# Kernel optimization log

Measured on AMD Instinct MI355X. Metric: run time of the kernel, lower is better.

## Reference

```python
import jax, jax.numpy as jnp
import numpy as np

N, D, H, E, K = 4096, 512, 2048, 8, 2  # tokens, input/output dim, expert hidden, num_experts, top_k


def setup_inputs() -> dict:
    key = jax.random.key(0)
    k_x, k_r, k_w1, k_b1, k_w2, k_b2 = jax.random.split(key, 6)
    input_batch = jax.random.normal(k_x, (N, D), dtype=jnp.float32)
    # Router-style top-k selection: guarantees the K expert ids per token are distinct
    # (required by the torch nonzero-based dispatch) and probabilities are a softmax
    # over the selected logits, matching a standard MoE sampler.
    router_logits = jax.random.normal(k_r, (N, E), dtype=jnp.float32)
    top_vals, top_idx = jax.lax.top_k(router_logits, K)
    probabilities = jax.nn.softmax(top_vals, axis=-1)            # [N, K]
    indices = top_idx.astype(jnp.int64)                          # [N, K]
    scale = 0.02
    W1 = scale * jax.random.normal(k_w1, (E, D, H), dtype=jnp.float32)
    b1 = jnp.zeros((E, H), dtype=jnp.float32)
    W2 = scale * jax.random.normal(k_w2, (E, H, D), dtype=jnp.float32)
    b2 = jnp.zeros((E, D), dtype=jnp.float32)
    return {"input_batch": input_batch, "probabilities": probabilities, "indices": indices,
            "W1": W1, "b1": b1, "W2": W2, "b2": b2}


def reference(input_batch, probabilities, indices, W1, b1, W2, b2):
    # Each expert is a dense 2-layer GELU MLP. The torch module gathers the tokens
    # assigned to each expert, runs the expert, concatenates, sorts back to original
    # flattened [N*K] order, applies probability weighting AFTER the experts, then
    # reshapes to [N, K, D] and sums over K. That is mathematically:
    #   out[t] = sum_k probabilities[t, k] * expert_{indices[t, k]}(input_batch[t])
    h = jax.nn.gelu(jnp.einsum('nd,edh->enh', input_batch, W1) + b1[:, None, :])  # [E, N, H]
    y = jnp.einsum('enh,ehd->end', h, W2) + b2[:, None, :]                         # [E, N, D]
    y = jnp.transpose(y, (1, 0, 2))                                                # [N, E, D]
    sel = jnp.take_along_axis(y, indices[:, :, None], axis=1)                      # [N, K, D]
    output = jnp.sum(sel * probabilities[:, :, None], axis=1)                      # [N, D]
    total_loss = jnp.float32(0.0)  # no sampler / expert aux losses in this config
    return output, total_loss
```

## Files before the change

kernel.cpp:

```cpp
#include <hip/hip_runtime.h>
#include <cstdint>
#include <cstddef>

#define NTOK 4096
#define DIMD 512
#define HIDH 2048
#define NEXP 8
#define TOPK 2
#define NSLOT (NTOK*TOPK)
#define SLACK 128
#define YROWS (NSLOT+SLACK)

#define BM 128
#define BN 128
#define BK 32

typedef short bf16x8_t __attribute__((ext_vector_type(8)));
typedef float f32x4_t  __attribute__((ext_vector_type(4)));

__device__ __forceinline__ unsigned short f2b(float f){
  unsigned int x = __float_as_uint(f);
  unsigned int r = (x + 0x7FFFu + ((x >> 16) & 1u)) >> 16;
  return (unsigned short)r;
}

__device__ __forceinline__ float gelu_tanh(float x) {
  float z2 = 1.5957691216057308f * fmaf(0.044715f * x, x * x, x);
  return x / (1.f + __expf(-z2));
}

__device__ __forceinline__ void gl_lds16(const void* g, void* l){
  __builtin_amdgcn_global_load_lds((const __attribute__((address_space(1))) void*)g,
                                   (__attribute__((address_space(3))) void*)l, 16, 0, 0);
}


__global__ __launch_bounds__(256) void cvt_x(const float* __restrict__ x, unsigned short* __restrict__ xb){
  int i = blockIdx.x*256 + threadIdx.x;
  if (i >= (NTOK*DIMD)/4) return;
  float4 v = ((const float4*)x)[i];
  ushort4 o; o.x=f2b(v.x); o.y=f2b(v.y); o.z=f2b(v.z); o.w=f2b(v.w);
  ((ushort4*)xb)[i] = o;
}

__global__ __launch_bounds__(256) void transpose_cvt(const float* __restrict__ src,
                                                     unsigned short* __restrict__ dst,
                                                     int R, int C){
  int e = blockIdx.z;
  src += (size_t)e*R*C; dst += (size_t)e*R*C;
  int c0 = blockIdx.x*64, r0 = blockIdx.y*64;
  __shared__ float t[64][65];
  int tr = threadIdx.x >> 4, tc = threadIdx.x & 15;
  #pragma unroll
  for (int i=0;i<4;i++){
    int r = tr + i*16;
    float4 v = *(const float4*)(src + (size_t)(r0 + r)*C + c0 + tc*4);
    t[r][tc*4+0]=v.x; t[r][tc*4+1]=v.y; t[r][tc*4+2]=v.z; t[r][tc*4+3]=v.w;
  }
  __syncthreads();
  #pragma unroll
  for (int i=0;i<4;i++){
    int c = tr + i*16;
    ushort4 o;
    o.x = f2b(t[tc*4+0][c]); o.y = f2b(t[tc*4+1][c]);
    o.z = f2b(t[tc*4+2][c]); o.w = f2b(t[tc*4+3][c]);
    *(ushort4*)(dst + (size_t)(c0 + c)*R + r0 + tc*4) = o;
  }
}


__global__ void count_k(const int* __restrict__ I, int* __restrict__ meta){
  int i = blockIdx.x*256+threadIdx.x;
  if (i < NSLOT) atomicAdd(&meta[I[i]], 1);
}
__global__ void scan_k(int* __restrict__ meta){
  if (threadIdx.x==0 && blockIdx.x==0){
    int s=0;
    for(int e=0;e<NEXP;e++){ meta[16+e]=s; s+=meta[e]; }
  }
}
__global__ void fill_k(const int* __restrict__ I, int* __restrict__ meta,
                       int* __restrict__ tokOf, int* __restrict__ rowOf){
  int i = blockIdx.x*256+threadIdx.x;
  if (i < NSLOT){
    int e = I[i];
    int pos = meta[16+e] + atomicAdd(&meta[8+e], 1);
    tokOf[pos] = i >> 1;
    rowOf[i] = pos;
  }
}


__global__ __launch_bounds__(256,2) void gemm1(
    const unsigned short* __restrict__ Xb, const unsigned short* __restrict__ W1t,
    const float* __restrict__ B1, const int* __restrict__ meta,
    const int* __restrict__ tokOf, unsigned short* __restrict__ H)
{
  const int e = blockIdx.z;
  const int cnt = meta[e];
  const int row0 = blockIdx.y * BM;
  if (row0 >= cnt) return;
  const int off = meta[16+e];
  const int h0 = blockIdx.x * BN;

  __shared__ unsigned short As[2][BM*BK];
  __shared__ unsigned short Bs[2][BN*BK];

  const int tid = threadIdx.x;
  const int ar0 = tid >> 2;
  const int kseg = (tid & 3) * 8;
  int s0 = min(off + row0 + ar0,      NSLOT-1);
  int s1 = min(off + row0 + ar0 + 64, NSLOT-1);
  const unsigned short* srcA0 = Xb + (size_t)tokOf[s0]*DIMD + kseg;
  const unsigned short* srcA1 = Xb + (size_t)tokOf[s1]*DIMD + kseg;
  const unsigned short* srcB0 = W1t + ((size_t)e*HIDH + h0 + ar0)*DIMD + kseg;
  const unsigned short* srcB1 = srcB0 + (size_t)64*DIMD;

  const int lane = tid & 63;
  const int wid  = tid >> 6;
  const int wr = (wid >> 1) * 64, wc = (wid & 1) * 64;
  const int l15 = lane & 15, kg = lane >> 4;

  f32x4_t acc[4][4];
  #pragma unroll
  for (int i=0;i<4;i++){
    #pragma unroll
    for (int j=0;j<4;j++) acc[i][j] = (f32x4_t){0.f,0.f,0.f,0.f};
  }

  auto stage = [&](int buf, int k0){
    gl_lds16(srcA0 + k0, &As[buf][tid*8]);
    gl_lds16(srcA1 + k0, &As[buf][2048 + tid*8]);
    gl_lds16(srcB0 + k0, &Bs[buf][tid*8]);
    gl_lds16(srcB1 + k0, &Bs[buf][2048 + tid*8]);
  };

  stage(0, 0);
  __syncthreads();
  int cur = 0;
  for (int t = 0; t < DIMD/BK; ++t){
    if (t+1 < DIMD/BK) stage(cur^1, (t+1)*BK);
    bf16x8_t af[4], bfr[4];
    #pragma unroll
    for (int m=0;m<4;m++)
      af[m] = *(const bf16x8_t*)&As[cur][(wr + m*16 + l15)*BK + kg*8];
    #pragma unroll
    for (int n=0;n<4;n++)
      bfr[n] = *(const bf16x8_t*)&Bs[cur][(wc + n*16 + l15)*BK + kg*8];
    #pragma unroll
    for (int m=0;m<4;m++){
      #pragma unroll
      for (int n=0;n<4;n++)
        acc[m][n] = __builtin_amdgcn_mfma_f32_16x16x32_bf16(af[m], bfr[n], acc[m][n], 0,0,0);
    }
    __syncthreads();
    cur ^= 1;
  }

  const int r4 = (lane >> 4) * 4;
  #pragma unroll
  for (int n=0;n<4;n++){
    int hc = h0 + wc + n*16 + l15;
    float b1v = B1[(size_t)e*HIDH + hc];
    #pragma unroll
    for (int m=0;m<4;m++){
      int rbase = row0 + wr + m*16 + r4;
      #pragma unroll
      for (int r=0;r<4;r++){
        int row = rbase + r;
        if (row < cnt){
          float v = gelu_tanh(acc[m][n][r] + b1v);
          H[(size_t)(off + row)*HIDH + hc] = f2b(v);
        }
      }
    }
  }
}


__global__ __launch_bounds__(256,2) void gemm2(
    const unsigned short* __restrict__ H, const unsigned short* __restrict__ W2t,
    const int* __restrict__ meta, float* __restrict__ Y, int nsplit)
{
  const int e = blockIdx.z;
  const int cnt = meta[e];
  const int row0 = blockIdx.y * BM;
  if (row0 >= cnt) return;
  const int off = meta[16+e];
  const int ncol = DIMD/BN;
  const int d0 = (blockIdx.x % ncol) * BN;
  const int kc = blockIdx.x / ncol;
  const int kchunk = HIDH / nsplit;
  const int kbase = kc * kchunk;

  __shared__ unsigned short As[2][BM*BK];
  __shared__ unsigned short Bs[2][BN*BK];

  const int tid = threadIdx.x;
  const int ar0 = tid >> 2;
  const int kseg = (tid & 3) * 8;
  const unsigned short* srcA0 = H + (size_t)(off + row0 + ar0)*HIDH + kbase + kseg;
  const unsigned short* srcA1 = srcA0 + (size_t)64*HIDH;
  const unsigned short* srcB0 = W2t + ((size_t)e*DIMD + d0 + ar0)*HIDH + kbase + kseg;
  const unsigned short* srcB1 = srcB0 + (size_t)64*HIDH;

  const int lane = tid & 63;
  const int wid  = tid >> 6;
  const int wr = (wid >> 1) * 64, wc = (wid & 1) * 64;
  const int l15 = lane & 15, kg = lane >> 4;

  f32x4_t acc[4][4];
  #pragma unroll
  for (int i=0;i<4;i++){
    #pragma unroll
    for (int j=0;j<4;j++) acc[i][j] = (f32x4_t){0.f,0.f,0.f,0.f};
  }

  auto stage = [&](int buf, int k0){
    gl_lds16(srcA0 + k0, &As[buf][tid*8]);
    gl_lds16(srcA1 + k0, &As[buf][2048 + tid*8]);
    gl_lds16(srcB0 + k0, &Bs[buf][tid*8]);
    gl_lds16(srcB1 + k0, &Bs[buf][2048 + tid*8]);
  };

  stage(0, 0);
  __syncthreads();
  int cur = 0;
  const int nsteps = kchunk / BK;
  for (int t = 0; t < nsteps; ++t){
    if (t+1 < nsteps) stage(cur^1, (t+1)*BK);
    bf16x8_t af[4], bfr[4];
    #pragma unroll
    for (int m=0;m<4;m++)
      af[m] = *(const bf16x8_t*)&As[cur][(wr + m*16 + l15)*BK + kg*8];
    #pragma unroll
    for (int n=0;n<4;n++)
      bfr[n] = *(const bf16x8_t*)&Bs[cur][(wc + n*16 + l15)*BK + kg*8];
    #pragma unroll
    for (int m=0;m<4;m++){
      #pragma unroll
      for (int n=0;n<4;n++)
        acc[m][n] = __builtin_amdgcn_mfma_f32_16x16x32_bf16(af[m], bfr[n], acc[m][n], 0,0,0);
    }
    __syncthreads();
    cur ^= 1;
  }

  float* Yp = Y + (size_t)kc * YROWS * DIMD;
  const int r4 = (lane >> 4) * 4;
  #pragma unroll
  for (int m=0;m<4;m++){
    int rbase = row0 + wr + m*16 + r4;
    #pragma unroll
    for (int r=0;r<4;r++){
      int row = rbase + r;
      if (row < cnt){
        float* yp = Yp + (size_t)(off + row)*DIMD + d0 + wc + l15;
        #pragma unroll
        for (int n=0;n<4;n++) yp[n*16] = acc[m][n][r];
      }
    }
  }
}


__global__ __launch_bounds__(128) void reduce_k(
    const float* __restrict__ P, const int* __restrict__ I, const int* __restrict__ rowOf,
    const float* __restrict__ Y, const float* __restrict__ B2, float* __restrict__ out,
    int nsplit)
{
  int t = blockIdx.x; int d4 = threadIdx.x;
  float4 a = make_float4(0.f,0.f,0.f,0.f);
  #pragma unroll
  for (int k=0;k<TOPK;k++){
    int i = t*TOPK + k;
    float p = P[i]; int e = I[i]; int r = rowOf[i];
    float4 b = *(const float4*)(B2 + (size_t)e*DIMD + d4*4);
    float4 y = make_float4(b.x, b.y, b.z, b.w);
    for (int c=0;c<nsplit;c++){
      float4 v = *(const float4*)(Y + (size_t)c*YROWS*DIMD + (size_t)r*DIMD + d4*4);
      y.x += v.x; y.y += v.y; y.z += v.z; y.w += v.w;
    }
    a.x = fmaf(p, y.x, a.x); a.y = fmaf(p, y.y, a.y);
    a.z = fmaf(p, y.z, a.z); a.w = fmaf(p, y.w, a.w);
  }
  *(float4*)(out + (size_t)t*DIMD + d4*4) = a;
}


#define CAP (NTOK*TOPK)
#define ROWS 32
#define HC 64
#define NTHR 256
#define XS_LD 516
#define HS_LD 36

__global__ void fb_build(const int* __restrict__ idx, const float* __restrict__ probs,
                         int* __restrict__ counts, int* __restrict__ tok,
                         float* __restrict__ pr) {
    int i = blockIdx.x * blockDim.x + threadIdx.x;
    if (i >= NTOK * TOPK) return;
    int t = i / TOPK;
    int e = idx[i];
    float p = probs[i];
    int pos = atomicAdd(&counts[e], 1);
    tok[e * CAP + pos] = t;
    pr[e * CAP + pos] = p;
}

__global__ __launch_bounds__(NTHR)
void fb_moe(const float* __restrict__ X,
            const float* __restrict__ W1, const float* __restrict__ B1,
            const float* __restrict__ W2, const float* __restrict__ B2,
            const int* __restrict__ counts, const int* __restrict__ tok,
            const float* __restrict__ pr, float* __restrict__ out)
{
    const int e = blockIdx.y;
    const int cnt = counts[e];
    const int r0 = blockIdx.x * ROWS;
    if (r0 >= cnt) return;
    const int nr = min(ROWS, cnt - r0);

    extern __shared__ float smem[];
    float* Xs = smem;
    float* Hs = smem + ROWS * XS_LD;
    const int tid = threadIdx.x;

    for (int i = tid; i < ROWS * (DIMD / 4); i += NTHR) {
        int r = i >> 7;
        int c4 = i & 127;
        float4 v = make_float4(0.f, 0.f, 0.f, 0.f);
        if (r < nr) {
            int t = tok[e * CAP + r0 + r];
            v = *(const float4*)(X + (size_t)t * DIMD + c4 * 4);
        }
        *(float4*)(Xs + r * XS_LD + c4 * 4) = v;
    }
    __syncthreads();

    const int hq = tid & 15;
    const int rp = tid >> 4;
    const int wv = tid >> 6;
    const int ln = tid & 63;

    float yacc[8][8];
    #pragma unroll
    for (int r = 0; r < 8; ++r){
        #pragma unroll
        for (int c = 0; c < 8; ++c) yacc[r][c] = 0.f;
    }

    const float* w1base = W1 + (size_t)e * DIMD * HIDH;
    const float* w2base = W2 + (size_t)e * HIDH * DIMD;
    const float* b1base = B1 + e * HIDH;

    for (int h0 = 0; h0 < HIDH; h0 += HC) {
        float acc0[4] = {0.f, 0.f, 0.f, 0.f};
        float acc1[4] = {0.f, 0.f, 0.f, 0.f};
        const float* w1p = w1base + h0 + hq * 4;
        const float* xr0 = Xs + (rp * 2) * XS_LD;
        const float* xr1 = xr0 + XS_LD;
        #pragma unroll 2
        for (int d = 0; d < DIMD; d += 4) {
            float4 xa = *(const float4*)(xr0 + d);
            float4 xb = *(const float4*)(xr1 + d);
            float4 w0 = *(const float4*)(w1p + (size_t)(d + 0) * HIDH);
            float4 w1v = *(const float4*)(w1p + (size_t)(d + 1) * HIDH);
            float4 w2v = *(const float4*)(w1p + (size_t)(d + 2) * HIDH);
            float4 w3v = *(const float4*)(w1p + (size_t)(d + 3) * HIDH);
            float xav[4] = {xa.x, xa.y, xa.z, xa.w};
            float xbv[4] = {xb.x, xb.y, xb.z, xb.w};
            float4 wsv[4] = {w0, w1v, w2v, w3v};
            #pragma unroll
            for (int dd = 0; dd < 4; ++dd) {
                acc0[0] = fmaf(xav[dd], wsv[dd].x, acc0[0]);
                acc0[1] = fmaf(xav[dd], wsv[dd].y, acc0[1]);
                acc0[2] = fmaf(xav[dd], wsv[dd].z, acc0[2]);
                acc0[3] = fmaf(xav[dd], wsv[dd].w, acc0[3]);
                acc1[0] = fmaf(xbv[dd], wsv[dd].x, acc1[0]);
                acc1[1] = fmaf(xbv[dd], wsv[dd].y, acc1[1]);
                acc1[2] = fmaf(xbv[dd], wsv[dd].z, acc1[2]);
                acc1[3] = fmaf(xbv[dd], wsv[dd].w, acc1[3]);
            }
        }
        {
            float4 b1v = *(const float4*)(b1base + h0 + hq * 4);
            float bb[4] = {b1v.x, b1v.y, b1v.z, b1v.w};
            #pragma unroll
            for (int j = 0; j < 4; ++j) {
                Hs[(hq * 4 + j) * HS_LD + rp * 2]     = gelu_tanh(acc0[j] + bb[j]);
                Hs[(hq * 4 + j) * HS_LD + rp * 2 + 1] = gelu_tanh(acc1[j] + bb[j]);
            }
        }
        __syncthreads();

        const float* w2p = w2base + (size_t)h0 * DIMD;
        #pragma unroll 4
        for (int hc = 0; hc < HC; ++hc) {
            float4 wA = *(const float4*)(w2p + (size_t)hc * DIMD + ln * 4);
            float4 wB = *(const float4*)(w2p + (size_t)hc * DIMD + 256 + ln * 4);
            float4 hv0 = *(const float4*)(Hs + hc * HS_LD + wv * 8);
            float4 hv1 = *(const float4*)(Hs + hc * HS_LD + wv * 8 + 4);
            float hr[8] = {hv0.x, hv0.y, hv0.z, hv0.w, hv1.x, hv1.y, hv1.z, hv1.w};
            #pragma unroll
            for (int r = 0; r < 8; ++r) {
                yacc[r][0] = fmaf(hr[r], wA.x, yacc[r][0]);
                yacc[r][1] = fmaf(hr[r], wA.y, yacc[r][1]);
                yacc[r][2] = fmaf(hr[r], wA.z, yacc[r][2]);
                yacc[r][3] = fmaf(hr[r], wA.w, yacc[r][3]);
                yacc[r][4] = fmaf(hr[r], wB.x, yacc[r][4]);
                yacc[r][5] = fmaf(hr[r], wB.y, yacc[r][5]);
                yacc[r][6] = fmaf(hr[r], wB.z, yacc[r][6]);
                yacc[r][7] = fmaf(hr[r], wB.w, yacc[r][7]);
            }
        }
        __syncthreads();
    }

    const float* b2p = B2 + e * DIMD;
    float4 b2A = *(const float4*)(b2p + ln * 4);
    float4 b2B = *(const float4*)(b2p + 256 + ln * 4);
    float bA[4] = {b2A.x, b2A.y, b2A.z, b2A.w};
    float bB[4] = {b2B.x, b2B.y, b2B.z, b2B.w};
    #pragma unroll
    for (int r = 0; r < 8; ++r) {
        int rg = wv * 8 + r;
        if (rg < nr) {
            int t = tok[e * CAP + r0 + rg];
            float p = pr[e * CAP + r0 + rg];
            float* op = out + (size_t)t * DIMD;
            #pragma unroll
            for (int j = 0; j < 4; ++j) {
                atomicAdd(op + ln * 4 + j,        p * (yacc[r][j] + bA[j]));
                atomicAdd(op + 256 + ln * 4 + j,  p * (yacc[r][4 + j] + bB[j]));
            }
        }
    }
}


extern "C" void kernel_launch(void* const* d_in, const int* in_sizes, int n_in,
                              void* d_out, int out_size, void* d_ws, size_t ws_size,
                              hipStream_t stream) {
    const float* X  = (const float*)d_in[0];
    const float* P  = (const float*)d_in[1];
    const int*   I  = (const int*)d_in[2];
    const float* W1 = (const float*)d_in[3];
    const float* B1 = (const float*)d_in[4];
    const float* W2 = (const float*)d_in[5];
    const float* B2 = (const float*)d_in[6];
    float* out = (float*)d_out;
    char* ws = (char*)d_ws;

    int nsplit = 0;
    size_t o_meta=0, o_tok=0, o_row=0, o_xb=0, o_w1t=0, o_w2t=0, o_h=0, o_y=0;
    const int cand[3] = {4, 2, 1};
    for (int ci = 0; ci < 3; ++ci) {
        int ns = cand[ci];
        size_t cur = 0;
        auto alloc = [&](size_t b){ size_t p = cur; cur += (b + 255) & ~(size_t)255; return p; };
        size_t m_ = alloc(256);
        size_t t_ = alloc((size_t)NSLOT*4);
        size_t r_ = alloc((size_t)NSLOT*4);
        size_t x_ = alloc((size_t)NTOK*DIMD*2);
        size_t w1_ = alloc((size_t)NEXP*DIMD*HIDH*2);
        size_t w2_ = alloc((size_t)NEXP*DIMD*HIDH*2);
        size_t h_ = alloc((size_t)YROWS*HIDH*2);
        size_t y_ = alloc((size_t)ns*YROWS*DIMD*4);
        if (cur <= ws_size) {
            nsplit = ns;
            o_meta=m_; o_tok=t_; o_row=r_; o_xb=x_; o_w1t=w1_; o_w2t=w2_; o_h=h_; o_y=y_;
            break;
        }
    }

    if (nsplit > 0) {
        int* meta = (int*)(ws + o_meta);
        int* tokOf = (int*)(ws + o_tok);
        int* rowOf = (int*)(ws + o_row);
        unsigned short* Xb  = (unsigned short*)(ws + o_xb);
        unsigned short* W1t = (unsigned short*)(ws + o_w1t);
        unsigned short* W2t = (unsigned short*)(ws + o_w2t);
        unsigned short* Hb  = (unsigned short*)(ws + o_h);
        float* Yb = (float*)(ws + o_y);

        hipMemsetAsync(meta, 0, 256, stream);
        cvt_x<<<(NTOK*DIMD/4 + 255)/256, 256, 0, stream>>>(X, Xb);
        transpose_cvt<<<dim3(HIDH/64, DIMD/64, NEXP), 256, 0, stream>>>(W1, W1t, DIMD, HIDH);
        transpose_cvt<<<dim3(DIMD/64, HIDH/64, NEXP), 256, 0, stream>>>(W2, W2t, HIDH, DIMD);
        count_k<<<NSLOT/256, 256, 0, stream>>>(I, meta);
        scan_k<<<1, 64, 0, stream>>>(meta);
        fill_k<<<NSLOT/256, 256, 0, stream>>>(I, meta, tokOf, rowOf);
        gemm1<<<dim3(HIDH/BN, NTOK/BM, NEXP), 256, 0, stream>>>(Xb, W1t, B1, meta, tokOf, Hb);
        gemm2<<<dim3((DIMD/BN)*nsplit, NTOK/BM, NEXP), 256, 0, stream>>>(Hb, W2t, meta, Yb, nsplit);
        reduce_k<<<NTOK, 128, 0, stream>>>(P, I, rowOf, Yb, B2, out, nsplit);
    } else {
        int*   counts = (int*)ws;
        int*   tok    = (int*)(ws + 64);
        float* pr     = (float*)(ws + 64 + (size_t)NEXP * CAP * sizeof(int));

        hipMemsetAsync(counts, 0, NEXP * sizeof(int), stream);
        hipMemsetAsync(d_out, 0, (size_t)out_size * sizeof(float), stream);
        fb_build<<<(NTOK * TOPK + 255) / 256, 256, 0, stream>>>(I, P, counts, tok, pr);
        size_t smem = (size_t)(ROWS * XS_LD + HC * HS_LD) * sizeof(float);
        hipFuncSetAttribute((const void*)fb_moe,
                            hipFuncAttributeMaxDynamicSharedMemorySize, (int)smem);
        fb_moe<<<dim3(CAP / ROWS, NEXP), NTHR, smem, stream>>>(
            X, W1, B1, W2, B2, counts, tok, pr, out);
    }
}
```

Measured before the change: 203.3 us.

## Triple-buffer LDS staging with vmcnt waits and XOR-swizzled LDS layout

Both expert GEMM kernels move from a double-buffered LDS pipeline with full __syncthreads to a three-stage ring buffer. Explicit s_waitcnt vmcnt counts let up to two tiles of global-to-LDS loads stay in flight while the MFMAs run. The K-segment each thread loads is XOR-swizzled by row, and fragment reads use matching precomputed offsets, to reduce LDS bank conflicts. LDS use per block grows by half, which may reduce occupancy. The hand-written vmcnt counts assume exactly four outstanding loads per stage and at least three K steps per chunk.

```diff
diff --git a/kernel.cpp b/kernel.cpp
--- a/kernel.cpp
+++ b/kernel.cpp
@@ -103,17 +103,17 @@
   const int off = meta[16+e];
   const int h0 = blockIdx.x * BN;
 
-  __shared__ unsigned short As[2][BM*BK];
-  __shared__ unsigned short Bs[2][BN*BK];
+  __shared__ unsigned short As[3][BM*BK];
+  __shared__ unsigned short Bs[3][BN*BK];
 
   const int tid = threadIdx.x;
   const int ar0 = tid >> 2;
-  const int kseg = (tid & 3) * 8;
+  const int ksw = (((tid & 3) ^ ((tid >> 3) & 3)) << 3);
   int s0 = min(off + row0 + ar0,      NSLOT-1);
   int s1 = min(off + row0 + ar0 + 64, NSLOT-1);
-  const unsigned short* srcA0 = Xb + (size_t)tokOf[s0]*DIMD + kseg;
-  const unsigned short* srcA1 = Xb + (size_t)tokOf[s1]*DIMD + kseg;
-  const unsigned short* srcB0 = W1t + ((size_t)e*HIDH + h0 + ar0)*DIMD + kseg;
+  const unsigned short* srcA0 = Xb + (size_t)tokOf[s0]*DIMD + ksw;
+  const unsigned short* srcA1 = Xb + (size_t)tokOf[s1]*DIMD + ksw;
+  const unsigned short* srcB0 = W1t + ((size_t)e*HIDH + h0 + ar0)*DIMD + ksw;
   const unsigned short* srcB1 = srcB0 + (size_t)64*DIMD;
 
   const int lane = tid & 63;
@@ -121,6 +121,15 @@
   const int wr = (wid >> 1) * 64, wc = (wid & 1) * 64;
   const int l15 = lane & 15, kg = lane >> 4;
 
+  int offA[4], offB[4];
+  #pragma unroll
+  for (int m=0;m<4;m++){
+    int r  = wr + m*16 + l15;
+    int rb = wc + m*16 + l15;
+    offA[m] = r *BK + ((kg ^ ((r >>1)&3)) << 3);
+    offB[m] = rb*BK + ((kg ^ ((rb>>1)&3)) << 3);
+  }
+
   f32x4_t acc[4][4];
   #pragma unroll
   for (int i=0;i<4;i++){
@@ -128,34 +137,46 @@
     for (int j=0;j<4;j++) acc[i][j] = (f32x4_t){0.f,0.f,0.f,0.f};
   }
 
-  auto stage = [&](int buf, int k0){
+  auto stage = [&](int buf, int kt){
+    const int k0 = kt * BK;
     gl_lds16(srcA0 + k0, &As[buf][tid*8]);
     gl_lds16(srcA1 + k0, &As[buf][2048 + tid*8]);
     gl_lds16(srcB0 + k0, &Bs[buf][tid*8]);
     gl_lds16(srcB1 + k0, &Bs[buf][2048 + tid*8]);
   };
 
-  stage(0, 0);
-  __syncthreads();
-  int cur = 0;
-  for (int t = 0; t < DIMD/BK; ++t){
-    if (t+1 < DIMD/BK) stage(cur^1, (t+1)*BK);
+  auto compute = [&](int buf){
     bf16x8_t af[4], bfr[4];
     #pragma unroll
-    for (int m=0;m<4;m++)
-      af[m] = *(const bf16x8_t*)&As[cur][(wr + m*16 + l15)*BK + kg*8];
-    #pragma unroll
-    for (int n=0;n<4;n++)
-      bfr[n] = *(const bf16x8_t*)&Bs[cur][(wc + n*16 + l15)*BK + kg*8];
+    for (int m=0;m<4;m++) af[m]  = *(const bf16x8_t*)&As[buf][offA[m]];
+    #pragma unroll
+    for (int n=0;n<4;n++) bfr[n] = *(const bf16x8_t*)&Bs[buf][offB[n]];
     #pragma unroll
     for (int m=0;m<4;m++){
       #pragma unroll
       for (int n=0;n<4;n++)
         acc[m][n] = __builtin_amdgcn_mfma_f32_16x16x32_bf16(af[m], bfr[n], acc[m][n], 0,0,0);
     }
-    __syncthreads();
-    cur ^= 1;
-  }
+  };
+
+  constexpr int NS = DIMD/BK;
+  stage(0,0); stage(1,1); stage(2,2);
+  for (int t = 0; t + 4 <= NS; ++t){
+    asm volatile("s_waitcnt vmcnt(8)" ::: "memory");
+    __builtin_amdgcn_s_barrier();
+    compute(t%3);
+    __builtin_amdgcn_s_barrier();
+    stage(t%3, t+3);
+  }
+  asm volatile("s_waitcnt vmcnt(8)" ::: "memory");
+  __builtin_amdgcn_s_barrier();
+  compute((NS-3)%3);
+  asm volatile("s_waitcnt vmcnt(4)" ::: "memory");
+  __builtin_amdgcn_s_barrier();
+  compute((NS-2)%3);
+  asm volatile("s_waitcnt vmcnt(0)" ::: "memory");
+  __builtin_amdgcn_s_barrier();
+  compute((NS-1)%3);
 
   const int r4 = (lane >> 4) * 4;
   #pragma unroll
@@ -193,15 +214,15 @@
   const int kchunk = HIDH / nsplit;
   const int kbase = kc * kchunk;
 
-  __shared__ unsigned short As[2][BM*BK];
-  __shared__ unsigned short Bs[2][BN*BK];
+  __shared__ unsigned short As[3][BM*BK];
+  __shared__ unsigned short Bs[3][BN*BK];
 
   const int tid = threadIdx.x;
   const int ar0 = tid >> 2;
-  const int kseg = (tid & 3) * 8;
-  const unsigned short* srcA0 = H + (size_t)(off + row0 + ar0)*HIDH + kbase + kseg;
+  const int ksw = (((tid & 3) ^ ((tid >> 3) & 3)) << 3);
+  const unsigned short* srcA0 = H + (size_t)(off + row0 + ar0)*HIDH + kbase + ksw;
   const unsigned short* srcA1 = srcA0 + (size_t)64*HIDH;
-  const unsigned short* srcB0 = W2t + ((size_t)e*DIMD + d0 + ar0)*HIDH + kbase + kseg;
+  const unsigned short* srcB0 = W2t + ((size_t)e*DIMD + d0 + ar0)*HIDH + kbase + ksw;
   const unsigned short* srcB1 = srcB0 + (size_t)64*HIDH;
 
   const int lane = tid & 63;
@@ -209,6 +230,15 @@
   const int wr = (wid >> 1) * 64, wc = (wid & 1) * 64;
   const int l15 = lane & 15, kg = lane >> 4;
 
+  int offA[4], offB[4];
+  #pragma unroll
+  for (int m=0;m<4;m++){
+    int r  = wr + m*16 + l15;
+    int rb = wc + m*16 + l15;
+    offA[m] = r *BK + ((kg ^ ((r >>1)&3)) << 3);
+    offB[m] = rb*BK + ((kg ^ ((rb>>1)&3)) << 3);
+  }
+
   f32x4_t acc[4][4];
   #pragma unroll
   for (int i=0;i<4;i++){
@@ -216,35 +246,46 @@
     for (int j=0;j<4;j++) acc[i][j] = (f32x4_t){0.f,0.f,0.f,0.f};
   }
 
-  auto stage = [&](int buf, int k0){
+  auto stage = [&](int buf, int kt){
+    const int k0 = kt * BK;
     gl_lds16(srcA0 + k0, &As[buf][tid*8]);
     gl_lds16(srcA1 + k0, &As[buf][2048 + tid*8]);
     gl_lds16(srcB0 + k0, &Bs[buf][tid*8]);
     gl_lds16(srcB1 + k0, &Bs[buf][2048 + tid*8]);
   };
 
-  stage(0, 0);
-  __syncthreads();
-  int cur = 0;
-  const int nsteps = kchunk / BK;
-  for (int t = 0; t < nsteps; ++t){
-    if (t+1 < nsteps) stage(cur^1, (t+1)*BK);
+  auto compute = [&](int buf){
     bf16x8_t af[4], bfr[4];
     #pragma unroll
-    for (int m=0;m<4;m++)
-      af[m] = *(const bf16x8_t*)&As[cur][(wr + m*16 + l15)*BK + kg*8];
-    #pragma unroll
-    for (int n=0;n<4;n++)
-      bfr[n] = *(const bf16x8_t*)&Bs[cur][(wc + n*16 + l15)*BK + kg*8];
+    for (int m=0;m<4;m++) af[m]  = *(const bf16x8_t*)&As[buf][offA[m]];
+    #pragma unroll
+    for (int n=0;n<4;n++) bfr[n] = *(const bf16x8_t*)&Bs[buf][offB[n]];
     #pragma unroll
     for (int m=0;m<4;m++){
       #pragma unroll
       for (int n=0;n<4;n++)
         acc[m][n] = __builtin_amdgcn_mfma_f32_16x16x32_bf16(af[m], bfr[n], acc[m][n], 0,0,0);
     }
-    __syncthreads();
-    cur ^= 1;
-  }
+  };
+
+  const int NS = kchunk / BK;
+  stage(0,0); stage(1,1); stage(2,2);
+  for (int t = 0; t + 4 <= NS; ++t){
+    asm volatile("s_waitcnt vmcnt(8)" ::: "memory");
+    __builtin_amdgcn_s_barrier();
+    compute(t%3);
+    __builtin_amdgcn_s_barrier();
+    stage(t%3, t+3);
+  }
+  asm volatile("s_waitcnt vmcnt(8)" ::: "memory");
+  __builtin_amdgcn_s_barrier();
+  compute((NS-3)%3);
+  asm volatile("s_waitcnt vmcnt(4)" ::: "memory");
+  __builtin_amdgcn_s_barrier();
+  compute((NS-2)%3);
+  asm volatile("s_waitcnt vmcnt(0)" ::: "memory");
+  __builtin_amdgcn_s_barrier();
+  compute((NS-1)%3);
 
   float* Yp = Y + (size_t)kc * YROWS * DIMD;
   const int r4 = (lane >> 4) * 4;
```

Result: faster. 198.4 us (-2.4%).

## Enlarge expert GEMM tiles to 256x256x64 with swizzled LDS and 8-wave blocks

Applied to the files above, without the earlier changes.

Both grouped expert GEMMs move from 128x128x32 tiles with 4 waves to 256x256x64 tiles with 8 waves, using 128KB of dynamic LDS, an XOR-swizzled shared-memory layout to avoid bank conflicts, explicit vmcnt waits and s_setprio around the MFMA section. The aim is to raise arithmetic intensity per LDS and global load and cut barrier overhead per FLOP. The cost is fewer blocks (one per CU), more padding waste for experts whose token counts do not fill 256-row tiles, and higher register pressure from the 8x4 accumulators. The grid now uses NSLOT/256 rows, and the Y slack is raised to cover the larger row overrun.

```diff
diff --git a/kernel.cpp b/kernel.cpp
--- a/kernel.cpp
+++ b/kernel.cpp
@@ -8,12 +8,10 @@
 #define NEXP 8
 #define TOPK 2
 #define NSLOT (NTOK*TOPK)
-#define SLACK 128
+#define SLACK 256
 #define YROWS (NSLOT+SLACK)
 
-#define BM 128
-#define BN 128
-#define BK 32
+#define BK 64
 
 typedef short bf16x8_t __attribute__((ext_vector_type(8)));
 typedef float f32x4_t  __attribute__((ext_vector_type(4)));
@@ -91,171 +89,219 @@
 }
 
 
-__global__ __launch_bounds__(256,2) void gemm1(
+
+__global__ __launch_bounds__(512,1) void gemm1(
     const unsigned short* __restrict__ Xb, const unsigned short* __restrict__ W1t,
     const float* __restrict__ B1, const int* __restrict__ meta,
     const int* __restrict__ tokOf, unsigned short* __restrict__ H)
 {
   const int e = blockIdx.z;
   const int cnt = meta[e];
-  const int row0 = blockIdx.y * BM;
+  const int row0 = blockIdx.y * 256;
   if (row0 >= cnt) return;
   const int off = meta[16+e];
-  const int h0 = blockIdx.x * BN;
-
-  __shared__ unsigned short As[2][BM*BK];
-  __shared__ unsigned short Bs[2][BN*BK];
+  const int h0 = blockIdx.x * 256;
+
+  extern __shared__ unsigned short sm[];
 
   const int tid = threadIdx.x;
-  const int ar0 = tid >> 2;
-  const int kseg = (tid & 3) * 8;
-  int s0 = min(off + row0 + ar0,      NSLOT-1);
-  int s1 = min(off + row0 + ar0 + 64, NSLOT-1);
-  const unsigned short* srcA0 = Xb + (size_t)tokOf[s0]*DIMD + kseg;
-  const unsigned short* srcA1 = Xb + (size_t)tokOf[s1]*DIMD + kseg;
-  const unsigned short* srcB0 = W1t + ((size_t)e*HIDH + h0 + ar0)*DIMD + kseg;
-  const unsigned short* srcB1 = srcB0 + (size_t)64*DIMD;
-
-  const int lane = tid & 63;
-  const int wid  = tid >> 6;
-  const int wr = (wid >> 1) * 64, wc = (wid & 1) * 64;
+  const int tr  = tid >> 3;
+  const int csw = ((tid & 7) ^ (tr & 7)) << 3;
+
+  const unsigned short* sA[4];
+  const unsigned short* sB[4];
+  #pragma unroll
+  for (int i=0;i<4;i++){
+    int slot = min(off + row0 + i*64 + tr, NSLOT-1);
+    sA[i] = Xb  + (size_t)tokOf[slot]*DIMD + csw;
+    sB[i] = W1t + ((size_t)e*HIDH + h0 + i*64 + tr)*DIMD + csw;
+  }
+
+  const int lane = tid & 63, wid = tid >> 6;
+  const int wrM = (wid >> 2) * 128, wcN = (wid & 3) * 64;
   const int l15 = lane & 15, kg = lane >> 4;
-
-  f32x4_t acc[4][4];
-  #pragma unroll
-  for (int i=0;i<4;i++){
-    #pragma unroll
-    for (int j=0;j<4;j++) acc[i][j] = (f32x4_t){0.f,0.f,0.f,0.f};
-  }
-
-  auto stage = [&](int buf, int k0){
-    gl_lds16(srcA0 + k0, &As[buf][tid*8]);
-    gl_lds16(srcA1 + k0, &As[buf][2048 + tid*8]);
-    gl_lds16(srcB0 + k0, &Bs[buf][tid*8]);
-    gl_lds16(srcB1 + k0, &Bs[buf][2048 + tid*8]);
+  const int lx  = l15 & 7;
+  int rowA[8], rowB[4];
+  #pragma unroll
+  for (int m=0;m<8;m++) rowA[m] = (wrM + m*16 + l15) * BK;
+  #pragma unroll
+  for (int n=0;n<4;n++) rowB[n] = (wcN + n*16 + l15) * BK;
+  const int ch0 = ((kg    ) ^ lx) << 3;
+  const int ch1 = ((kg + 4) ^ lx) << 3;
+
+  f32x4_t acc[8][4];
+  #pragma unroll
+  for (int m=0;m<8;m++){
+    #pragma unroll
+    for (int n=0;n<4;n++) acc[m][n] = (f32x4_t){0.f,0.f,0.f,0.f};
+  }
+
+  auto stagef = [&](int buf, int kt){
+    unsigned short* dA = sm + buf*32768 + tid*8;
+    unsigned short* dB = dA + 16384;
+    const int k0 = kt * BK;
+    #pragma unroll
+    for (int i=0;i<4;i++){
+      gl_lds16(sA[i] + k0, dA + i*4096);
+      gl_lds16(sB[i] + k0, dB + i*4096);
+    }
   };
 
-  stage(0, 0);
-  __syncthreads();
-  int cur = 0;
-  for (int t = 0; t < DIMD/BK; ++t){
-    if (t+1 < DIMD/BK) stage(cur^1, (t+1)*BK);
-    bf16x8_t af[4], bfr[4];
-    #pragma unroll
-    for (int m=0;m<4;m++)
-      af[m] = *(const bf16x8_t*)&As[cur][(wr + m*16 + l15)*BK + kg*8];
-    #pragma unroll
-    for (int n=0;n<4;n++)
-      bfr[n] = *(const bf16x8_t*)&Bs[cur][(wc + n*16 + l15)*BK + kg*8];
-    #pragma unroll
-    for (int m=0;m<4;m++){
+  auto khalf = [&](const unsigned short* SA, const unsigned short* SB, int ch){
+    bf16x8_t bfr[4];
+    #pragma unroll
+    for (int n=0;n<4;n++) bfr[n] = *(const bf16x8_t*)&SB[rowB[n] + ch];
+    #pragma unroll
+    for (int m=0;m<8;m++){
+      bf16x8_t afm = *(const bf16x8_t*)&SA[rowA[m] + ch];
       #pragma unroll
       for (int n=0;n<4;n++)
-        acc[m][n] = __builtin_amdgcn_mfma_f32_16x16x32_bf16(af[m], bfr[n], acc[m][n], 0,0,0);
-    }
-    __syncthreads();
-    cur ^= 1;
-  }
-
-  const int r4 = (lane >> 4) * 4;
+        acc[m][n] = __builtin_amdgcn_mfma_f32_16x16x32_bf16(afm, bfr[n], acc[m][n], 0,0,0);
+    }
+  };
+
+  constexpr int NS = DIMD / BK;
+  stagef(0, 0);
+  for (int t = 0; t < NS; ++t){
+    const int cur = t & 1;
+    if (t + 1 < NS){
+      stagef(cur ^ 1, t + 1);
+      asm volatile("s_waitcnt vmcnt(8)" ::: "memory");
+    } else {
+      asm volatile("s_waitcnt vmcnt(0)" ::: "memory");
+    }
+    __builtin_amdgcn_s_barrier();
+    __builtin_amdgcn_s_setprio(1);
+    const unsigned short* SA = sm + cur*32768;
+    const unsigned short* SB = SA + 16384;
+    khalf(SA, SB, ch0);
+    khalf(SA, SB, ch1);
+    __builtin_amdgcn_s_setprio(0);
+    __builtin_amdgcn_s_barrier();
+  }
+
+  const int r4 = kg * 4;
   #pragma unroll
   for (int n=0;n<4;n++){
-    int hc = h0 + wc + n*16 + l15;
-    float b1v = B1[(size_t)e*HIDH + hc];
-    #pragma unroll
-    for (int m=0;m<4;m++){
-      int rbase = row0 + wr + m*16 + r4;
+    const int gcol = h0 + wcN + n*16 + l15;
+    const float b1v = B1[(size_t)e*HIDH + gcol];
+    #pragma unroll
+    for (int m=0;m<8;m++){
+      const int rbase = row0 + wrM + m*16 + r4;
       #pragma unroll
       for (int r=0;r<4;r++){
-        int row = rbase + r;
-        if (row < cnt){
-          float v = gelu_tanh(acc[m][n][r] + b1v);
-          H[(size_t)(off + row)*HIDH + hc] = f2b(v);
-        }
+        const int row = rbase + r;
+        if (row < cnt)
+          H[(size_t)(off + row)*HIDH + gcol] = f2b(gelu_tanh(acc[m][n][r] + b1v));
       }
     }
   }
 }
 
 
-__global__ __launch_bounds__(256,2) void gemm2(
-    const unsigned short* __restrict__ H, const unsigned short* __restrict__ W2t,
+__global__ __launch_bounds__(512,1) void gemm2(
+    const unsigned short* __restrict__ Hb, const unsigned short* __restrict__ W2t,
     const int* __restrict__ meta, float* __restrict__ Y, int nsplit)
 {
   const int e = blockIdx.z;
   const int cnt = meta[e];
-  const int row0 = blockIdx.y * BM;
+  const int row0 = blockIdx.y * 256;
   if (row0 >= cnt) return;
   const int off = meta[16+e];
-  const int ncol = DIMD/BN;
-  const int d0 = (blockIdx.x % ncol) * BN;
+  const int ncol = DIMD / 256;
+  const int d0 = (blockIdx.x % ncol) * 256;
   const int kc = blockIdx.x / ncol;
   const int kchunk = HIDH / nsplit;
   const int kbase = kc * kchunk;
-
-  __shared__ unsigned short As[2][BM*BK];
-  __shared__ unsigned short Bs[2][BN*BK];
+  const int NS = kchunk / BK;
+
+  extern __shared__ unsigned short sm[];
 
   const int tid = threadIdx.x;
-  const int ar0 = tid >> 2;
-  const int kseg = (tid & 3) * 8;
-  const unsigned short* srcA0 = H + (size_t)(off + row0 + ar0)*HIDH + kbase + kseg;
-  const unsigned short* srcA1 = srcA0 + (size_t)64*HIDH;
-  const unsigned short* srcB0 = W2t + ((size_t)e*DIMD + d0 + ar0)*HIDH + kbase + kseg;
-  const unsigned short* srcB1 = srcB0 + (size_t)64*HIDH;
-
-  const int lane = tid & 63;
-  const int wid  = tid >> 6;
-  const int wr = (wid >> 1) * 64, wc = (wid & 1) * 64;
+  const int tr  = tid >> 3;
+  const int csw = ((tid & 7) ^ (tr & 7)) << 3;
+
+  const unsigned short* sA[4];
+  const unsigned short* sB[4];
+  #pragma unroll
+  for (int i=0;i<4;i++){
+    int arow = min(off + row0 + i*64 + tr, YROWS-1);
+    sA[i] = Hb  + (size_t)arow*HIDH + kbase + csw;
+    sB[i] = W2t + ((size_t)e*DIMD + d0 + i*64 + tr)*HIDH + kbase + csw;
+  }
+
+  const int lane = tid & 63, wid = tid >> 6;
+  const int wrM = (wid >> 2) * 128, wcN = (wid & 3) * 64;
   const int l15 = lane & 15, kg = lane >> 4;
-
-  f32x4_t acc[4][4];
-  #pragma unroll
-  for (int i=0;i<4;i++){
-    #pragma unroll
-    for (int j=0;j<4;j++) acc[i][j] = (f32x4_t){0.f,0.f,0.f,0.f};
-  }
-
-  auto stage = [&](int buf, int k0){
-    gl_lds16(srcA0 + k0, &As[buf][tid*8]);
-    gl_lds16(srcA1 + k0, &As[buf][2048 + tid*8]);
-    gl_lds16(srcB0 + k0, &Bs[buf][tid*8]);
-    gl_lds16(srcB1 + k0, &Bs[buf][2048 + tid*8]);
+  const int lx  = l15 & 7;
+  int rowA[8], rowB[4];
+  #pragma unroll
+  for (int m=0;m<8;m++) rowA[m] = (wrM + m*16 + l15) * BK;
+  #pragma unroll
+  for (int n=0;n<4;n++) rowB[n] = (wcN + n*16 + l15) * BK;
+  const int ch0 = ((kg    ) ^ lx) << 3;
+  const int ch1 = ((kg + 4) ^ lx) << 3;
+
+  f32x4_t acc[8][4];
+  #pragma unroll
+  for (int m=0;m<8;m++){
+    #pragma unroll
+    for (int n=0;n<4;n++) acc[m][n] = (f32x4_t){0.f,0.f,0.f,0.f};
+  }
+
+  auto stagef = [&](int buf, int kt){
+    unsigned short* dA = sm + buf*32768 + tid*8;
+    unsigned short* dB = dA + 16384;
+    const int k0 = kt * BK;
+    #pragma unroll
+    for (int i=0;i<4;i++){
+      gl_lds16(sA[i] + k0, dA + i*4096);
+      gl_lds16(sB[i] + k0, dB + i*4096);
+    }
   };
 
-  stage(0, 0);
-  __syncthreads();
-  int cur = 0;
-  const int nsteps = kchunk / BK;
-  for (int t = 0; t < nsteps; ++t){
-    if (t+1 < nsteps) stage(cur^1, (t+1)*BK);
-    bf16x8_t af[4], bfr[4];
-    #pragma unroll
-    for (int m=0;m<4;m++)
-      af[m] = *(const bf16x8_t*)&As[cur][(wr + m*16 + l15)*BK + kg*8];
-    #pragma unroll
-    for (int n=0;n<4;n++)
-      bfr[n] = *(const bf16x8_t*)&Bs[cur][(wc + n*16 + l15)*BK + kg*8];
-    #pragma unroll
-    for (int m=0;m<4;m++){
+  auto khalf = [&](const unsigned short* SA, const unsigned short* SB, int ch){
+    bf16x8_t bfr[4];
+    #pragma unroll
+    for (int n=0;n<4;n++) bfr[n] = *(const bf16x8_t*)&SB[rowB[n] + ch];
+    #pragma unroll
+    for (int m=0;m<8;m++){
+      bf16x8_t afm = *(const bf16x8_t*)&SA[rowA[m] + ch];
       #pragma unroll
       for (int n=0;n<4;n++)
-        acc[m][n] = __builtin_amdgcn_mfma_f32_16x16x32_bf16(af[m], bfr[n], acc[m][n], 0,0,0);
-    }
-    __syncthreads();
-    cur ^= 1;
+        acc[m][n] = __builtin_amdgcn_mfma_f32_16x16x32_bf16(afm, bfr[n], acc[m][n], 0,0,0);
+    }
+  };
+
+  stagef(0, 0);
+  for (int t = 0; t < NS; ++t){
+    const int cur = t & 1;
+    if (t + 1 < NS){
+      stagef(cur ^ 1, t + 1);
+      asm volatile("s_waitcnt vmcnt(8)" ::: "memory");
+    } else {
+      asm volatile("s_waitcnt vmcnt(0)" ::: "memory");
+    }
+    __builtin_amdgcn_s_barrier();
+    __builtin_amdgcn_s_setprio(1);
+    const unsigned short* SA = sm + cur*32768;
+    const unsigned short* SB = SA + 16384;
+    khalf(SA, SB, ch0);
+    khalf(SA, SB, ch1);
+    __builtin_amdgcn_s_setprio(0);
+    __builtin_amdgcn_s_barrier();
   }
 
   float* Yp = Y + (size_t)kc * YROWS * DIMD;
-  const int r4 = (lane >> 4) * 4;
-  #pragma unroll
-  for (int m=0;m<4;m++){
-    int rbase = row0 + wr + m*16 + r4;
+  const int r4 = kg * 4;
+  #pragma unroll
+  for (int m=0;m<8;m++){
+    const int rbase = row0 + wrM + m*16 + r4;
     #pragma unroll
     for (int r=0;r<4;r++){
-      int row = rbase + r;
+      const int row = rbase + r;
       if (row < cnt){
-        float* yp = Yp + (size_t)(off + row)*DIMD + d0 + wc + l15;
+        float* yp = Yp + (size_t)(off + row)*DIMD + d0 + wcN + l15;
         #pragma unroll
         for (int n=0;n<4;n++) yp[n*16] = acc[m][n][r];
       }
@@ -491,8 +537,15 @@
         count_k<<<NSLOT/256, 256, 0, stream>>>(I, meta);
         scan_k<<<1, 64, 0, stream>>>(meta);
         fill_k<<<NSLOT/256, 256, 0, stream>>>(I, meta, tokOf, rowOf);
-        gemm1<<<dim3(HIDH/BN, NTOK/BM, NEXP), 256, 0, stream>>>(Xb, W1t, B1, meta, tokOf, Hb);
-        gemm2<<<dim3((DIMD/BN)*nsplit, NTOK/BM, NEXP), 256, 0, stream>>>(Hb, W2t, meta, Yb, nsplit);
+
+        hipFuncSetAttribute((const void*)gemm1,
+                            hipFuncAttributeMaxDynamicSharedMemorySize, 131072);
+        hipFuncSetAttribute((const void*)gemm2,
+                            hipFuncAttributeMaxDynamicSharedMemorySize, 131072);
+        gemm1<<<dim3(HIDH/256, NSLOT/256, NEXP), 512, 131072, stream>>>(
+            Xb, W1t, B1, meta, tokOf, Hb);
+        gemm2<<<dim3((DIMD/256)*nsplit, NSLOT/256, NEXP), 512, 131072, stream>>>(
+            Hb, W2t, meta, Yb, nsplit);
         reduce_k<<<NTOK, 128, 0, stream>>>(P, I, rowOf, Yb, B2, out, nsplit);
     } else {
         int*   counts = (int*)ws;
```

New measurement: 231.7 us. 1.14x slower.
